# Optimization experiments

Hardware: AMD Instinct MI355X
Metric: run time of the kernel (lower is better)

The kernel has to match this reference:

```python
import jax, jax.numpy as jnp
import numpy as np

B = 64            # batch
C = 2             # num_channels (BSF syndrome: X and Z)
L = 64            # lattice size
N = 16            # gradient (histogram) size
BIN = 360 // N    # bin_size = 22 degrees
EPS = 1e-5        # BatchNorm2d default eps


def setup_inputs() -> dict:
    key = jax.random.key(0)
    k1, = jax.random.split(key, 1)
    # syndrome in BSF: binary 0/1 values (torch.nonzero picks the set bits)
    x = jax.random.randint(k1, (B, C * L * L * L), 0, 2).astype(jnp.float32)
    gamma = jnp.ones((C,), jnp.float32)   # BatchNorm2d weight
    beta = jnp.zeros((C,), jnp.float32)   # BatchNorm2d bias
    return {"x": x, "gamma": gamma, "beta": beta}


def _bin_tables():
    # Per lattice site (i,j,k): magnitude and flattened (ax, az) bin index.
    c = jnp.arange(L, dtype=jnp.float32)
    i = c[:, None, None]
    j = c[None, :, None]
    k = c[None, None, :]
    mag = jnp.sqrt(i * i + j * j + k * k)          # (L,L,L)
    x_comp = jnp.sqrt(j * j + k * k)
    z_comp = jnp.sqrt(j * j + i * i)
    deg = 180.0 / jnp.pi
    # atan2 results are in [0, pi] here, so int() truncation == floor
    ax = jnp.floor(jnp.arctan2(x_comp, i) * deg / BIN).astype(jnp.int32)
    az = jnp.floor(jnp.arctan2(k, z_comp) * deg / BIN).astype(jnp.int32)
    bins = (ax * N + az).reshape(-1)               # (L^3,) flattened (ax,az)
    return mag.reshape(-1), bins


def reference(x, gamma, beta):
    mag, bins = _bin_tables()
    # torch.nonzero + indexed update == mask-weighted scatter of magnitudes.
    # x is 0/1, so x * mag equals the mags of the nonzero sites (0 elsewhere).
    xw = x.reshape(B, C, L * L * L) * mag                     # (B,C,L^3)
    g = jnp.zeros((B, C, N * N), x.dtype).at[:, :, bins].add(xw)
    g = g.reshape(B, C, N, N)
    # BatchNorm2d, training mode: per-channel batch statistics (biased var)
    mean = g.mean(axis=(0, 2, 3), keepdims=True)
    var = ((g - mean) ** 2).mean(axis=(0, 2, 3), keepdims=True)
    gn = (g - mean) * jax.lax.rsqrt(var + EPS)
    return gn * gamma[None, :, None, None] + beta[None, :, None, None]
```

## Files before the change

### kernel.cpp

```cpp
#include <hip/hip_runtime.h>


#define BINS_PAD 80
#define SLOTS 10

__global__ __launch_bounds__(256)
void bin_table_kernel(unsigned char* __restrict__ tab, float* __restrict__ g) {
    int v = blockIdx.x * 256 + threadIdx.x;
    int i = v >> 12, j = (v >> 6) & 63, k = v & 63;
    double xc2 = (double)(j * j + k * k);
    double zc2 = (double)(i * i + j * j);
    double i2  = (double)(i * i);
    double k2  = (double)(k * k);
    const double T1 = 0.4040262258351568  * 0.4040262258351568;
    const double T2 = 0.9656887748070740  * 0.9656887748070740;
    const double T3 = 2.2460367739042161  * 2.2460367739042161;
    const double T4 = 28.636253282915602  * 28.636253282915602;
    int ax = (xc2 > i2 * T1) + (xc2 > i2 * T2) + (xc2 > i2 * T3) + (xc2 > i2 * T4);
    int az = (k2 > zc2 * T1) + (k2 > zc2 * T2) + (k2 > zc2 * T3) + (k2 > zc2 * T4);
    tab[v] = (unsigned char)(ax * 16 + az);
    if (v < 32768) g[v] = 0.0f;
}

__global__ __launch_bounds__(256)
void scatter_kernel(const float4* __restrict__ x4,
                    const uint4* __restrict__ tab4,
                    float* __restrict__ g) {
    __shared__ unsigned long long slot[256][SLOTS];
    __shared__ float hist[BINS_PAD];
    int tid = threadIdx.x;
    int p   = blockIdx.x >> 6;
    int i   = blockIdx.x & 63;

    const unsigned long long SENT = ((unsigned long long)69u) << 32;
    #pragma unroll
    for (int s = 0; s < SLOTS; ++s) slot[tid][s] = SENT;
    if (tid < BINS_PAD) hist[tid] = 0.0f;

    int j  = tid >> 2;
    int k0 = (tid & 3) * 16;

    const float4* xs = x4 + (size_t)p * 65536 + (size_t)i * 1024;
    uint4  tb = tab4[i * 256 + tid];
    float4 xq0 = xs[4 * tid + 0];
    float4 xq1 = xs[4 * tid + 1];
    float4 xq2 = xs[4 * tid + 2];
    float4 xq3 = xs[4 * tid + 3];

    float r2f = (float)(i * i + j * j);

    float4       xq[4] = {xq0, xq1, xq2, xq3};
    unsigned int uq[4] = {tb.x, tb.y, tb.z, tb.w};

    int   cnt  = -1;
    int   prev = -1;
    float acc  = 0.0f;
    unsigned long long* myslot = slot[tid];

    #pragma unroll
    for (int q = 0; q < 4; ++q) {
        unsigned int u = uq[q];
        #pragma unroll
        for (int e = 0; e < 4; ++e) {
            float k   = (float)(k0 + 4 * q + e);
            float xe  = (e == 0) ? xq[q].x : (e == 1) ? xq[q].y : (e == 2) ? xq[q].z : xq[q].w;
            float val = xe * sqrtf(fmaf(k, k, r2f));
            int   b   = (u >> (8 * e)) & 255;
            bool  ch  = (b != prev);
            cnt += ch ? 1 : 0;
            acc  = ch ? val : (acc + val);
            prev = b;
            myslot[cnt] = (((unsigned long long)(unsigned)b) << 32)
                        | (unsigned long long)__float_as_uint(acc);
        }
    }
    __syncthreads();

    #pragma unroll
    for (int s = 0; s < SLOTS; ++s) {
        unsigned long long pk = myslot[s];
        float av = __uint_as_float((unsigned int)pk);
        if (av != 0.0f) {
            unsigned int bb = (unsigned int)(pk >> 32);
            atomicAdd(&hist[bb], av);
        }
    }
    __syncthreads();

    if (tid < BINS_PAD) {
        float hv = hist[tid];
        if (hv != 0.0f) atomicAdd(&g[p * 256 + tid], hv);
    }
}

__global__ __launch_bounds__(1024)
void norm_kernel(const float* __restrict__ g,
                 const float* __restrict__ gamma,
                 const float* __restrict__ beta,
                 float* __restrict__ out) {
    __shared__ double red[16][4];
    __shared__ float  coef[4];
    int t = threadIdx.x;
    float vals[32];
    double s0 = 0.0, s1 = 0.0, q0 = 0.0, q1 = 0.0;
    #pragma unroll
    for (int n = 0; n < 32; ++n) {
        int idx = t + n * 1024;
        float v = g[idx];
        vals[n] = v;
        double vd = (double)v;
        if ((idx >> 8) & 1) { s1 += vd; q1 += vd * vd; }
        else                { s0 += vd; q0 += vd * vd; }
    }
    #pragma unroll
    for (int off = 32; off > 0; off >>= 1) {
        s0 += __shfl_down(s0, off);
        s1 += __shfl_down(s1, off);
        q0 += __shfl_down(q0, off);
        q1 += __shfl_down(q1, off);
    }
    int wave = t >> 6;
    if ((t & 63) == 0) {
        red[wave][0] = s0; red[wave][1] = s1; red[wave][2] = q0; red[wave][3] = q1;
    }
    __syncthreads();
    if (t == 0) {
        double S0 = 0, S1 = 0, Q0 = 0, Q1 = 0;
        for (int wv = 0; wv < 16; ++wv) {
            S0 += red[wv][0]; S1 += red[wv][1]; Q0 += red[wv][2]; Q1 += red[wv][3];
        }
        const double inv_n = 1.0 / 16384.0;
        double m0 = S0 * inv_n, m1 = S1 * inv_n;
        double v0 = Q0 * inv_n - m0 * m0;
        double v1 = Q1 * inv_n - m1 * m1;
        double r0 = 1.0 / sqrt(v0 + 1e-5);
        double r1 = 1.0 / sqrt(v1 + 1e-5);
        float g0 = gamma[0], g1 = gamma[1], b0 = beta[0], b1 = beta[1];
        coef[0] = (float)r0 * g0;
        coef[1] = (float)r1 * g1;
        coef[2] = b0 - (float)(m0 * r0) * g0;
        coef[3] = b1 - (float)(m1 * r1) * g1;
    }
    __syncthreads();
    float sc0 = coef[0], sc1 = coef[1], sh0 = coef[2], sh1 = coef[3];
    #pragma unroll
    for (int n = 0; n < 32; ++n) {
        int idx = t + n * 1024;
        int c = (idx >> 8) & 1;
        out[idx] = vals[n] * (c ? sc1 : sc0) + (c ? sh1 : sh0);
    }
}

extern "C" void kernel_launch(void* const* d_in, const int* in_sizes, int n_in,
                              void* d_out, int out_size, void* d_ws, size_t ws_size,
                              hipStream_t stream) {
    const float* x     = (const float*)d_in[0];
    const float* gamma = (const float*)d_in[1];
    const float* beta  = (const float*)d_in[2];
    float* out = (float*)d_out;

    unsigned char* tab = (unsigned char*)d_ws;
    float*         g   = (float*)((char*)d_ws + 262144);

    bin_table_kernel<<<1024, 256, 0, stream>>>(tab, g);
    scatter_kernel<<<8192, 256, 0, stream>>>((const float4*)x, (const uint4*)tab, g);
    norm_kernel<<<1, 1024, 0, stream>>>(g, gamma, beta, out);
}
```

Before: 205.4 us.

## Process two batch-channel planes per scatter block and transpose slot storage

Each scatter block now handles two (batch,channel) planes that share the same lattice row, so the bin table load, magnitude sqrt and run-length segmentation are computed once and reused for both. The grid is halved to 4096 blocks. Slot arrays are transposed to [slot][thread] to avoid LDS bank conflicts, and the second plane's values are stored in a separate float array. This trades more registers and LDS per block, and so possibly lower occupancy, for less redundant work and fewer blocks.

```diff
diff --git a/kernel.cpp b/kernel.cpp
--- a/kernel.cpp
+++ b/kernel.cpp
@@ -26,70 +26,80 @@
 void scatter_kernel(const float4* __restrict__ x4,
                     const uint4* __restrict__ tab4,
                     float* __restrict__ g) {
-    __shared__ unsigned long long slot[256][SLOTS];
-    __shared__ float hist[BINS_PAD];
+    __shared__ unsigned long long slotA[SLOTS][256];
+    __shared__ float              slotB[SLOTS][256];
+    __shared__ float hist[2][BINS_PAD];
     int tid = threadIdx.x;
-    int p   = blockIdx.x >> 6;
+    int pA  = blockIdx.x >> 6;
+    int pB  = pA + 64;
     int i   = blockIdx.x & 63;
 
     const unsigned long long SENT = ((unsigned long long)69u) << 32;
     #pragma unroll
-    for (int s = 0; s < SLOTS; ++s) slot[tid][s] = SENT;
-    if (tid < BINS_PAD) hist[tid] = 0.0f;
+    for (int s = 0; s < SLOTS; ++s) { slotA[s][tid] = SENT; slotB[s][tid] = 0.0f; }
+    if (tid < 2 * BINS_PAD) ((float*)hist)[tid] = 0.0f;
 
     int j  = tid >> 2;
     int k0 = (tid & 3) * 16;
 
-    const float4* xs = x4 + (size_t)p * 65536 + (size_t)i * 1024;
+    const float4* xsA = x4 + (size_t)pA * 65536 + (size_t)i * 1024;
+    const float4* xsB = x4 + (size_t)pB * 65536 + (size_t)i * 1024;
     uint4  tb = tab4[i * 256 + tid];
-    float4 xq0 = xs[4 * tid + 0];
-    float4 xq1 = xs[4 * tid + 1];
-    float4 xq2 = xs[4 * tid + 2];
-    float4 xq3 = xs[4 * tid + 3];
+    float4 xqA[4], xqB[4];
+    #pragma unroll
+    for (int q = 0; q < 4; ++q) xqA[q] = xsA[4 * tid + q];
+    #pragma unroll
+    for (int q = 0; q < 4; ++q) xqB[q] = xsB[4 * tid + q];
 
     float r2f = (float)(i * i + j * j);
-
-    float4       xq[4] = {xq0, xq1, xq2, xq3};
     unsigned int uq[4] = {tb.x, tb.y, tb.z, tb.w};
 
     int   cnt  = -1;
     int   prev = -1;
-    float acc  = 0.0f;
-    unsigned long long* myslot = slot[tid];
+    float accA = 0.0f, accB = 0.0f;
 
     #pragma unroll
     for (int q = 0; q < 4; ++q) {
         unsigned int u = uq[q];
         #pragma unroll
         for (int e = 0; e < 4; ++e) {
-            float k   = (float)(k0 + 4 * q + e);
-            float xe  = (e == 0) ? xq[q].x : (e == 1) ? xq[q].y : (e == 2) ? xq[q].z : xq[q].w;
-            float val = xe * sqrtf(fmaf(k, k, r2f));
-            int   b   = (u >> (8 * e)) & 255;
-            bool  ch  = (b != prev);
+            float k    = (float)(k0 + 4 * q + e);
+            float mag  = sqrtf(fmaf(k, k, r2f));
+            float xeA  = (e == 0) ? xqA[q].x : (e == 1) ? xqA[q].y : (e == 2) ? xqA[q].z : xqA[q].w;
+            float xeB  = (e == 0) ? xqB[q].x : (e == 1) ? xqB[q].y : (e == 2) ? xqB[q].z : xqB[q].w;
+            float valA = xeA * mag;
+            float valB = xeB * mag;
+            int   b    = (u >> (8 * e)) & 255;
+            bool  ch   = (b != prev);
             cnt += ch ? 1 : 0;
-            acc  = ch ? val : (acc + val);
+            accA = ch ? valA : (accA + valA);
+            accB = ch ? valB : (accB + valB);
             prev = b;
-            myslot[cnt] = (((unsigned long long)(unsigned)b) << 32)
-                        | (unsigned long long)__float_as_uint(acc);
+            slotA[cnt][tid] = (((unsigned long long)(unsigned)b) << 32)
+                            | (unsigned long long)__float_as_uint(accA);
+            slotB[cnt][tid] = accB;
         }
     }
     __syncthreads();
 
     #pragma unroll
     for (int s = 0; s < SLOTS; ++s) {
-        unsigned long long pk = myslot[s];
+        unsigned long long pk = slotA[s][tid];
         float av = __uint_as_float((unsigned int)pk);
-        if (av != 0.0f) {
-            unsigned int bb = (unsigned int)(pk >> 32);
-            atomicAdd(&hist[bb], av);
-        }
+        float bv = slotB[s][tid];
+        unsigned int bb = (unsigned int)(pk >> 32);
+        if (av != 0.0f) atomicAdd(&hist[0][bb], av);
+        if (bv != 0.0f) atomicAdd(&hist[1][bb], bv);
     }
     __syncthreads();
 
     if (tid < BINS_PAD) {
-        float hv = hist[tid];
-        if (hv != 0.0f) atomicAdd(&g[p * 256 + tid], hv);
+        float hv = hist[0][tid];
+        if (hv != 0.0f) atomicAdd(&g[pA * 256 + tid], hv);
+    } else if (tid < 2 * BINS_PAD) {
+        int b2 = tid - BINS_PAD;
+        float hv = hist[1][b2];
+        if (hv != 0.0f) atomicAdd(&g[pB * 256 + b2], hv);
     }
 }
 
@@ -163,6 +173,6 @@
     float*         g   = (float*)((char*)d_ws + 262144);
 
     bin_table_kernel<<<1024, 256, 0, stream>>>(tab, g);
-    scatter_kernel<<<8192, 256, 0, stream>>>((const float4*)x, (const uint4*)tab, g);
+    scatter_kernel<<<4096, 256, 0, stream>>>((const float4*)x, (const uint4*)tab, g);
     norm_kernel<<<1, 1024, 0, stream>>>(g, gamma, beta, out);
 }
```

After: 207.3 us. About the same (+0.9%).
